# Kernel tuning notes

Measured on AMD Instinct MI355X. Metric: run time of the kernel, lower is better.

The kernel has to match this reference:

```python
import jax, jax.numpy as jnp
import numpy as np

D = 64      # hidden_dim
H = 4       # num_attention_heads
DH = D // H # head_dim
B = 64      # graphs per batch
SCALE = np.float32(np.sqrt(DH))


def _sage(x, edge, wl, bl, wr):
    # SAGEConv: lin_l(mean_j x_j) + lin_r(x_i); mean over incoming edges (dst = edge[1])
    src, dst = edge[0], edge[1]
    n = x.shape[0]
    agg = jax.ops.segment_sum(x[src], dst, num_segments=n)
    cnt = jax.ops.segment_sum(jnp.ones((edge.shape[1],), x.dtype), dst, num_segments=n)
    mean = agg / jnp.maximum(cnt, 1.0)[:, None]
    return mean @ wl + bl + x @ wr


def _cross_attn(xq, xk, w, b):
    # w: [3, D, D] stacked (Q, K, V) projections; b: [3, D]
    Q = (xq @ w[0] + b[0]).reshape(-1, H, DH)  # [Nq, H, DH]
    K = (xk @ w[1] + b[1]).reshape(-1, H, DH)  # [Nk, H, DH]
    V = (xk @ w[2] + b[2]).reshape(-1, H, DH)
    scores = jnp.einsum('qhd,khd->hqk', Q, K) / SCALE  # [H, Nq, Nk]
    wgt = jax.nn.softmax(scores, axis=-1)
    out = jnp.einsum('hqk,khd->qhd', wgt, V)
    return out.reshape(xq.shape[0], D)


def _segment_mean(x, seg, num):
    s = jax.ops.segment_sum(x, seg, num_segments=num)
    c = jax.ops.segment_sum(jnp.ones((x.shape[0],), x.dtype), seg, num_segments=num)
    return s / jnp.maximum(c, 1.0)[:, None]


def setup_inputs() -> dict:
    key = jax.random.key(0)
    ks = jax.random.split(key, 32)
    N_MOL, N_PROT, E_MOL, E_PROT = 2048, 8192, 32768, 131072
    MOL_IN, PROT_IN = 32, 64

    def lin(k, i, o, s=None):
        s = 1.0 / np.sqrt(i) if s is None else s
        return (jax.random.normal(k, (i, o), jnp.float32) * s)

    inp = {
        'x_mol': jax.random.normal(ks[0], (N_MOL, MOL_IN), jnp.float32),
        'x_prot': jax.random.normal(ks[1], (N_PROT, PROT_IN), jnp.float32),
        'm1_wl': lin(ks[2], MOL_IN, D), 'm1_bl': jnp.zeros((D,), jnp.float32), 'm1_wr': lin(ks[3], MOL_IN, D),
        'm2_wl': lin(ks[4], D, D), 'm2_bl': jnp.zeros((D,), jnp.float32), 'm2_wr': lin(ks[5], D, D),
        'p1_wl': lin(ks[6], PROT_IN, D), 'p1_bl': jnp.zeros((D,), jnp.float32), 'p1_wr': lin(ks[7], PROT_IN, D),
        'p2_wl': lin(ks[8], D, D), 'p2_bl': jnp.zeros((D,), jnp.float32), 'p2_wr': lin(ks[9], D, D),
        'amp_w': jax.random.normal(ks[10], (3, D, D), jnp.float32) / np.sqrt(D),
        'amp_b': jnp.zeros((3, D), jnp.float32),
        'apm_w': jax.random.normal(ks[11], (3, D, D), jnp.float32) / np.sqrt(D),
        'apm_b': jnp.zeros((3, D), jnp.float32),
        'fc1_w': lin(ks[12], 2 * D, D), 'fc1_b': jnp.zeros((D,), jnp.float32),
        'fc2_w': lin(ks[13], D, 1), 'fc2_b': jnp.zeros((1,), jnp.float32),
        'edge_mol': jax.random.randint(ks[14], (2, E_MOL), 0, N_MOL, jnp.int32),
        'edge_prot': jax.random.randint(ks[15], (2, E_PROT), 0, N_PROT, jnp.int32),
        'batch_mol': jnp.sort(jax.random.randint(ks[16], (N_MOL,), 0, B, jnp.int32)),
        'batch_prot': jnp.sort(jax.random.randint(ks[17], (N_PROT,), 0, B, jnp.int32)),
    }
    return inp


def reference(x_mol, x_prot,
              m1_wl, m1_bl, m1_wr, m2_wl, m2_bl, m2_wr,
              p1_wl, p1_bl, p1_wr, p2_wl, p2_bl, p2_wr,
              amp_w, amp_b, apm_w, apm_b,
              fc1_w, fc1_b, fc2_w, fc2_b,
              edge_mol, edge_prot, batch_mol, batch_prot):
    # two SAGE conv blocks per graph, ReLU after each (HeteroConv with one edge type)
    h_mol = jax.nn.relu(_sage(x_mol, edge_mol, m1_wl, m1_bl, m1_wr))
    h_mol = jax.nn.relu(_sage(h_mol, edge_mol, m2_wl, m2_bl, m2_wr))
    h_prot = jax.nn.relu(_sage(x_prot, edge_prot, p1_wl, p1_bl, p1_wr))
    h_prot = jax.nn.relu(_sage(h_prot, edge_prot, p2_wl, p2_bl, p2_wr))
    # cross attention (mol queries prot, prot queries mol) + residual
    h_mol_c = h_mol + _cross_attn(h_mol, h_prot, amp_w, amp_b)
    h_prot_c = h_prot + _cross_attn(h_prot, h_mol, apm_w, apm_b)
    # global mean pool per graph
    z_mol = _segment_mean(h_mol_c, batch_mol, B)    # [B, D]
    z_prot = _segment_mean(h_prot_c, batch_prot, B)  # [B, D]
    z = jnp.concatenate([z_mol, z_prot], axis=1)     # [B, 2D]
    x = jax.nn.relu(z @ fc1_w + fc1_b)
    out = jax.nn.sigmoid(x @ fc2_w + fc2_b)
    return out.squeeze(-1)  # [B]
```

## Files before the change

### kernel.cpp

```cpp
#include <hip/hip_runtime.h>
#include <math.h>

#define D 64
#define NB 64

typedef __attribute__((ext_vector_type(8))) short bf16x8;
typedef __attribute__((ext_vector_type(4))) float f32x4;
typedef __attribute__((ext_vector_type(16))) float f32x16;

#define M3(a, b, c) fmaxf(fmaxf((a), (b)), (c))

__device__ __forceinline__ unsigned short f2bf(float f) {
    unsigned u = __float_as_uint(f);
    u += 0x7FFF + ((u >> 16) & 1);
    return (unsigned short)(u >> 16);
}
__device__ __forceinline__ unsigned pk_bf16(float lo, float hi) {
    unsigned r;
    asm("v_cvt_pk_bf16_f32 %0, %1, %2" : "=v"(r) : "v"(lo), "v"(hi));
    return r;
}
__device__ __forceinline__ float fexp2(float x) {
    float r;
    asm("v_exp_f32 %0, %1" : "=v"(r) : "v"(x));
    return r;
}

__global__ void k_hist2(const int* __restrict__ em, int Em,
                        const int* __restrict__ ep, int Ep,
                        int* __restrict__ degm, int* __restrict__ degp) {
    int i = blockIdx.x * blockDim.x + threadIdx.x;
    if (i < Em) atomicAdd(&degm[em[Em + i]], 1);
    int j = i - Em;
    if (j >= 0 && j < Ep) atomicAdd(&degp[ep[Ep + j]], 1);
}

__global__ __launch_bounds__(256) void k_scan2(
        const int* __restrict__ degm, int Nm, int* __restrict__ rpm, int* __restrict__ curm,
        const int* __restrict__ degp, int Np, int* __restrict__ rpp, int* __restrict__ curp) {
    __shared__ int sdeg[8192];
    __shared__ int chunk[256];
    const int* deg = blockIdx.x ? degp : degm;
    int N = blockIdx.x ? Np : Nm;
    int* rowptr = blockIdx.x ? rpp : rpm;
    int* cursor = blockIdx.x ? curp : curm;
    int t = threadIdx.x;
    for (int i = t; i < N; i += 256) sdeg[i] = deg[i];
    __syncthreads();
    int C = (N + 255) / 256;
    int start = t * C;
    int sum = 0;
    for (int i = 0; i < C; ++i)
        if (start + i < N) sum += sdeg[start + i];
    chunk[t] = sum;
    __syncthreads();
    for (int ofs = 1; ofs < 256; ofs <<= 1) {
        int v = (t >= ofs) ? chunk[t - ofs] : 0;
        __syncthreads();
        chunk[t] += v;
        __syncthreads();
    }
    int base = (t == 0) ? 0 : chunk[t - 1];
    for (int i = 0; i < C && start + i < N; ++i) {
        rowptr[start + i] = base;
        cursor[start + i] = base;
        base += sdeg[start + i];
    }
    if (t == 255) rowptr[N] = base;
}

__global__ void k_scatter2(const int* __restrict__ em, int Em, int* __restrict__ curm,
                           int* __restrict__ csrm,
                           const int* __restrict__ ep, int Ep, int* __restrict__ curp,
                           int* __restrict__ csrp) {
    int i = blockIdx.x * blockDim.x + threadIdx.x;
    if (i < Em) {
        int s = em[i], d = em[Em + i];
        csrm[atomicAdd(&curm[d], 1)] = s;
    }
    int j = i - Em;
    if (j >= 0 && j < Ep) {
        int s = ep[j], d = ep[Ep + j];
        csrp[atomicAdd(&curp[d], 1)] = s;
    }
}

__global__ void k_bstart2(const int* __restrict__ bm, int Nm, int* __restrict__ bsM,
                          const int* __restrict__ bp, int Np, int* __restrict__ bsP) {
    int i = blockIdx.x * blockDim.x + threadIdx.x;
    if (i < Nm) {
        int cur = bm[i];
        int prev = (i == 0) ? -1 : bm[i - 1];
        for (int b = prev + 1; b <= cur; ++b) bsM[b] = i;
        if (i == Nm - 1)
            for (int b = cur + 1; b <= NB; ++b) bsM[b] = Nm;
    }
    int j = i - Nm;
    if (j >= 0 && j < Np) {
        int cur = bp[j];
        int prev = (j == 0) ? -1 : bp[j - 1];
        for (int b = prev + 1; b <= cur; ++b) bsP[b] = j;
        if (j == Np - 1)
            for (int b = cur + 1; b <= NB; ++b) bsP[b] = Np;
    }
}

template<int FIN>
__device__ __forceinline__ void gsage_body(
        const float* __restrict__ x, const int* __restrict__ rowptr,
        const int* __restrict__ csr, int N,
        const float* __restrict__ wl, const float* __restrict__ bl,
        const float* __restrict__ wr, float* __restrict__ out,
        int blk, float* __restrict__ swl, float* __restrict__ swr,
        float* __restrict__ sagg, float* __restrict__ sx) {
    for (int i = threadIdx.x; i < FIN * D; i += 256) { swl[i] = wl[i]; swr[i] = wr[i]; }
    int w = threadIdx.x >> 6;
    int lane = threadIdx.x & 63;
    int r = blk * 4 + w;
    if (r < N) {
        int e0 = rowptr[r], e1 = rowptr[r + 1];
        float inv = 1.0f / fmaxf((float)(e1 - e0), 1.0f);
        if (FIN == 64) {
            float a0 = 0.f, a1 = 0.f, a2 = 0.f, a3 = 0.f;
            int e = e0;
            for (; e + 3 < e1; e += 4) {
                a0 += x[(size_t)csr[e] * FIN + lane];
                a1 += x[(size_t)csr[e + 1] * FIN + lane];
                a2 += x[(size_t)csr[e + 2] * FIN + lane];
                a3 += x[(size_t)csr[e + 3] * FIN + lane];
            }
            for (; e < e1; ++e) a0 += x[(size_t)csr[e] * FIN + lane];
            sagg[w * 64 + lane] = ((a0 + a1) + (a2 + a3)) * inv;
            sx[w * 64 + lane] = x[(size_t)r * FIN + lane];
        } else {
            int f = lane & 31, half = lane >> 5;
            float a = 0.f;
            for (int e = e0 + half; e < e1; e += 2)
                a += x[(size_t)csr[e] * FIN + f];
            a += __shfl_xor(a, 32);
            if (half == 0) {
                sagg[w * 64 + f] = a * inv;
                sx[w * 64 + f] = x[(size_t)r * FIN + f];
            }
        }
    }
    __syncthreads();
    if (r >= N) return;
    int c = lane;
    float acc = bl[c];
    #pragma unroll 8
    for (int k = 0; k < FIN; ++k) {
        acc += sagg[w * 64 + k] * swl[k * D + c];
        acc += sx[w * 64 + k] * swr[k * D + c];
    }
    out[(size_t)r * D + c] = fmaxf(acc, 0.0f);
}

template<int FA, int FB>
__global__ __launch_bounds__(256) void k_gsage2(
        const float* __restrict__ xA, const int* __restrict__ rpA,
        const int* __restrict__ csrA, int NA,
        const float* __restrict__ wlA, const float* __restrict__ blA,
        const float* __restrict__ wrA, float* __restrict__ outA,
        const float* __restrict__ xB, const int* __restrict__ rpB,
        const int* __restrict__ csrB, int NB_,
        const float* __restrict__ wlB, const float* __restrict__ blB,
        const float* __restrict__ wrB, float* __restrict__ outB) {
    __shared__ float swl[64 * 64];
    __shared__ float swr[64 * 64];
    __shared__ float sagg[4 * 64];
    __shared__ float sx[4 * 64];
    int bA = NA / 4;
    if ((int)blockIdx.x < bA)
        gsage_body<FA>(xA, rpA, csrA, NA, wlA, blA, wrA, outA, blockIdx.x, swl, swr, sagg, sx);
    else
        gsage_body<FB>(xB, rpB, csrB, NB_, wlB, blB, wrB, outB, blockIdx.x - bA, swl, swr, sagg, sx);
}

__global__ __launch_bounds__(256) void k_qkv2(
        const float* __restrict__ xA, int NA, const float* __restrict__ xB, int NB_,
        const float* __restrict__ amp_w, const float* __restrict__ amp_b,
        const float* __restrict__ apm_w, const float* __restrict__ apm_b, float qs,
        unsigned short* __restrict__ QA, unsigned short* __restrict__ KA, unsigned short* __restrict__ VA,
        unsigned short* __restrict__ QB, unsigned short* __restrict__ KB, unsigned short* __restrict__ VB) {
    __shared__ float sq[D * D], sk[D * D], sv[D * D], sx[16 * D];
    int bA = NA / 16;
    const float *x, *wq, *bq, *wk, *bk, *wv, *bv;
    unsigned short *oq, *ok, *ov;
    int blk;
    if ((int)blockIdx.x < bA) {
        x = xA; blk = blockIdx.x;
        wq = amp_w;        bq = amp_b;
        wk = apm_w + 4096; bk = apm_b + 64;
        wv = apm_w + 8192; bv = apm_b + 128;
        oq = QA; ok = KA; ov = VA;
    } else {
        x = xB; blk = blockIdx.x - bA;
        wq = apm_w;        bq = apm_b;
        wk = amp_w + 4096; bk = amp_b + 64;
        wv = amp_w + 8192; bv = amp_b + 128;
        oq = QB; ok = KB; ov = VB;
    }
    for (int i = threadIdx.x; i < D * D; i += 256) { sq[i] = wq[i]; sk[i] = wk[i]; sv[i] = wv[i]; }
    int rbase = blk * 16;
    for (int i = threadIdx.x; i < 16 * D; i += 256) sx[i] = x[(size_t)rbase * D + i];
    __syncthreads();
    int c = threadIdx.x & 63;
    int r0 = (threadIdx.x >> 6) * 4;
    for (int rr = 0; rr < 4; ++rr) {
        int r = r0 + rr;
        float aq = bq[c], ak = bk[c], av = bv[c];
        #pragma unroll 8
        for (int k = 0; k < D; ++k) {
            float xv = sx[r * D + k];
            aq += xv * sq[k * D + c];
            ak += xv * sk[k * D + c];
            av += xv * sv[k * D + c];
        }
        size_t o = (size_t)(rbase + r) * D + c;
        oq[o] = f2bf(aq * qs);
        ok[o] = f2bf(ak);
        ov[o] = f2bf(av);
    }
}

__global__ void k_transp2(const unsigned short* __restrict__ inM, unsigned short* __restrict__ outM, int Nm,
                          const unsigned short* __restrict__ inP, unsigned short* __restrict__ outP, int Np) {
    __shared__ unsigned short tile[64][72];
    int bm = Nm >> 6;
    const unsigned short* in; unsigned short* out; int N;
    int blk = blockIdx.x;
    if (blk < bm) { in = inM; out = outM; N = Nm; }
    else { blk -= bm; in = inP; out = outP; N = Np; }
    int t = threadIdx.x;
    int rbase = blk * 64;
    {
        int r = t >> 2, c0 = (t & 3) * 16;
        const uint4* src = (const uint4*)(in + (size_t)(rbase + r) * 64 + c0);
        uint4 a = src[0], b = src[1];
        *(uint4*)(&tile[r][c0]) = a;
        *(uint4*)(&tile[r][c0 + 8]) = b;
    }
    __syncthreads();
    {
        int c = t >> 2, r0 = (t & 3) * 16;
        union { uint2 v2[4]; unsigned short s[16]; } u;
        #pragma unroll
        for (int i = 0; i < 16; ++i) u.s[i] = tile[r0 + i][c];
        int key0 = rbase + r0;
        int kc = key0 & ~31;
        int b16 = key0 & 16;
        unsigned short* op = out + (size_t)c * N;
        const int gmap[4] = {0, 8, 4, 12};
        #pragma unroll
        for (int b = 0; b < 4; ++b)
            *(uint2*)(op + kc + b16 + gmap[b]) = u.v2[b];
    }
    if (t < 8) {
        uint4 ones;
        ones.x = ones.y = ones.z = ones.w = 0x3F803F80u;
        *(uint4*)(out + (size_t)64 * N + rbase + t * 8) = ones;
    }
}

#define PVBLOCK(S, KB)                                                        \
    {                                                                         \
        float p[16];                                                          \
        _Pragma("unroll")                                                     \
        for (int i = 0; i < 16; ++i) p[i] = fexp2((S)[i]);                    \
        union { unsigned u[4]; bf16x8 v; } f1, f2;                            \
        f1.u[0] = pk_bf16(p[0], p[1]);   f1.u[1] = pk_bf16(p[2], p[3]);       \
        f1.u[2] = pk_bf16(p[4], p[5]);   f1.u[3] = pk_bf16(p[6], p[7]);       \
        f2.u[0] = pk_bf16(p[8], p[9]);   f2.u[1] = pk_bf16(p[10], p[11]);     \
        f2.u[2] = pk_bf16(p[12], p[13]); f2.u[3] = pk_bf16(p[14], p[15]);     \
        bf16x8 vb0 = *(const bf16x8*)(vbase + (KB) + half * 8);               \
        bf16x8 vb1 = *(const bf16x8*)(vbase + (KB) + 16 + half * 8);          \
        __builtin_amdgcn_s_setprio(1);                                        \
        o = __builtin_amdgcn_mfma_f32_32x32x16_bf16(f1.v, vb0, o, 0, 0, 0);   \
        o = __builtin_amdgcn_mfma_f32_32x32x16_bf16(f2.v, vb1, o, 0, 0, 0);   \
        __builtin_amdgcn_s_setprio(0);                                        \
    }

#define MAXTREE(cm, s0, s1)                                                   \
    {                                                                         \
        float c0 = M3(s0[0], s0[1], s0[2]);                                   \
        float c1 = M3(s0[3], s0[4], s0[5]);                                   \
        float c2 = M3(s0[6], s0[7], s0[8]);                                   \
        float c3 = M3(s0[9], s0[10], s0[11]);                                 \
        float c4 = M3(s0[12], s0[13], s0[14]);                                \
        float c5 = M3(s0[15], s1[0], s1[1]);                                  \
        float c6 = M3(s1[2], s1[3], s1[4]);                                   \
        float c7 = M3(s1[5], s1[6], s1[7]);                                   \
        float c8 = M3(s1[8], s1[9], s1[10]);                                  \
        float c9 = M3(s1[11], s1[12], s1[13]);                                \
        float ca = fmaxf(s1[14], s1[15]);                                     \
        float d0 = M3(c0, c1, c2);                                            \
        float d1 = M3(c3, c4, c5);                                            \
        float d2 = M3(c6, c7, c8);                                            \
        float d3 = M3(c9, ca, d0);                                            \
        cm = M3(d1, d2, d3);                                                  \
    }

__global__ __launch_bounds__(256) void k_attn2(
        const unsigned short* __restrict__ QmB, const unsigned short* __restrict__ KpB,
        const unsigned short* __restrict__ VpT, int Nm, int Np, int lsm,
        float* __restrict__ poM, float* __restrict__ pmM, float* __restrict__ plM,
        const unsigned short* __restrict__ QpB, const unsigned short* __restrict__ KmB,
        const unsigned short* __restrict__ VmT, int lsp,
        float* __restrict__ poP, float* __restrict__ pmP, float* __restrict__ plP) {
    const unsigned short *Q, *K, *Vt;
    int Nq, Nk, ls;
    float *po, *pm, *pl;
    if (blockIdx.y == 0) { Q = QmB; K = KpB; Vt = VpT; Nq = Nm; Nk = Np; ls = lsm; po = poM; pm = pmM; pl = plM; }
    else                 { Q = QpB; K = KmB; Vt = VmT; Nq = Np; Nk = Nm; ls = lsp; po = poP; pm = pmP; pl = plP; }
    int nqt = Nq >> 5;
    if ((int)blockIdx.x >= (nqt << ls)) return;
    const int qt = blockIdx.x >> ls;
    const int split = blockIdx.x & ((1 << ls) - 1);
    const int kchunk = Nk >> ls;
    const int h = threadIdx.x >> 6;
    const int lane = threadIdx.x & 63;
    const int cq = lane & 31;
    const int half = lane >> 5;
    const int h16 = h * 16;

    bf16x8 qb = *(const bf16x8*)(Q + ((size_t)(qt * 32 + cq) * D + h16 + half * 8));
    int drow = (cq < 16) ? (h16 + cq) : (cq == 16 ? 64 : h16 + 15);
    const unsigned short* vbase = Vt + (size_t)drow * Nk;

    f32x16 o, mC, zro;
    #pragma unroll
    for (int i = 0; i < 16; ++i) { o[i] = 0.f; zro[i] = 0.f; }
    float m;

    const int kstart = split * kchunk;
    {
        const int kb = kstart;
        bf16x8 ka0 = *(const bf16x8*)(K + ((size_t)(kb + cq) * D + h16 + half * 8));
        bf16x8 ka1 = *(const bf16x8*)(K + ((size_t)(kb + 32 + cq) * D + h16 + half * 8));
        f32x16 s0 = __builtin_amdgcn_mfma_f32_32x32x16_bf16(ka0, qb, zro, 0, 0, 0);
        f32x16 s1 = __builtin_amdgcn_mfma_f32_32x32x16_bf16(ka1, qb, zro, 0, 0, 0);
        float cm;
        MAXTREE(cm, s0, s1);
        #pragma unroll
        for (int off = 1; off < 64; off <<= 1) cm = fmaxf(cm, __shfl_xor(cm, off));
        m = cm;
        #pragma unroll
        for (int i = 0; i < 16; ++i) { s0[i] -= m; s1[i] -= m; mC[i] = -m; }
        PVBLOCK(s0, kb)
        PVBLOCK(s1, kb + 32)
    }
    for (int kb = kstart + 64; kb < kstart + kchunk; kb += 64) {
        bf16x8 ka0 = *(const bf16x8*)(K + ((size_t)(kb + cq) * D + h16 + half * 8));
        bf16x8 ka1 = *(const bf16x8*)(K + ((size_t)(kb + 32 + cq) * D + h16 + half * 8));
        f32x16 s0 = __builtin_amdgcn_mfma_f32_32x32x16_bf16(ka0, qb, mC, 0, 0, 0);
        f32x16 s1 = __builtin_amdgcn_mfma_f32_32x32x16_bf16(ka1, qb, mC, 0, 0, 0);
        float cm;
        MAXTREE(cm, s0, s1);
        if (__any(cm > 8.f)) {
            float cw = cm;
            #pragma unroll
            for (int off = 1; off < 64; off <<= 1) cw = fmaxf(cw, __shfl_xor(cw, off));
            float nm = fmaxf(m + cw, m);
            float sc = fexp2(m - nm);
            #pragma unroll
            for (int i = 0; i < 16; ++i) o[i] *= sc;
            float dl = nm - m;
            #pragma unroll
            for (int i = 0; i < 16; ++i) { s0[i] -= dl; s1[i] -= dl; mC[i] = -nm; }
            m = nm;
        }
        PVBLOCK(s0, kb)
        PVBLOCK(s1, kb + 32)
    }

    size_t pbase = (size_t)split * Nq + qt * 32;
    if (half == 0)
        pm[(pbase + cq) * 4 + h] = m;
    if (cq == 16) {
        #pragma unroll
        for (int r = 0; r < 16; ++r) {
            int qr = (r & 3) + 8 * (r >> 2) + 4 * half;
            pl[(pbase + qr) * 4 + h] = o[r];
        }
    }
    if (cq < 16) {
        #pragma unroll
        for (int r = 0; r < 16; ++r) {
            int qr = (r & 3) + 8 * (r >> 2) + 4 * half;
            po[(pbase + qr) * 64 + h16 + cq] = o[r];
        }
    }
}

template<int NS>
__device__ __forceinline__ void comb_body(
        const float* __restrict__ po, const float* __restrict__ pm,
        const float* __restrict__ pl, int Nq,
        const float* __restrict__ resid, float* __restrict__ outc, int i) {
    int q = i >> 4;
    int part = i & 15;
    int d0 = part * 4;
    int h = part >> 2;
    float pmv[NS], plv[NS];
    #pragma unroll
    for (int s = 0; s < NS; ++s) pmv[s] = pm[((size_t)s * Nq + q) * 4 + h];
    #pragma unroll
    for (int s = 0; s < NS; ++s) plv[s] = pl[((size_t)s * Nq + q) * 4 + h];
    float M = pmv[0];
    #pragma unroll
    for (int s = 1; s < NS; ++s) M = fmaxf(M, pmv[s]);
    float4 O = {0.f, 0.f, 0.f, 0.f};
    float L = 0.f;
    #pragma unroll
    for (int s = 0; s < NS; ++s) {
        float wgt = fexp2(pmv[s] - M);
        float4 pv = *(const float4*)(po + ((size_t)s * Nq + q) * 64 + d0);
        O.x += pv.x * wgt; O.y += pv.y * wgt; O.z += pv.z * wgt; O.w += pv.w * wgt;
        L += plv[s] * wgt;
    }
    float invL = 1.0f / L;
    float4 rv = *(const float4*)(resid + (size_t)q * 64 + d0);
    float4 res;
    res.x = rv.x + O.x * invL;
    res.y = rv.y + O.y * invL;
    res.z = rv.z + O.z * invL;
    res.w = rv.w + O.w * invL;
    *(float4*)(outc + (size_t)q * 64 + d0) = res;
}

template<int NSM, int NSP>
__global__ void k_comb2t(
        const float* __restrict__ poM, const float* __restrict__ pmM, const float* __restrict__ plM,
        int Nm, const float* __restrict__ residM, float* __restrict__ outM,
        const float* __restrict__ poP, const float* __restrict__ pmP, const float* __restrict__ plP,
        int Np, const float* __restrict__ residP, float* __restrict__ outP) {
    int idx = blockIdx.x * blockDim.x + threadIdx.x;
    int mtot = Nm * 16;
    if (idx < mtot)
        comb_body<NSM>(poM, pmM, plM, Nm, residM, outM, idx);
    else if (idx - mtot < Np * 16)
        comb_body<NSP>(poP, pmP, plP, Np, residP, outP, idx - mtot);
}

__global__ void k_comb2(
        const float* __restrict__ poM, const float* __restrict__ pmM, const float* __restrict__ plM,
        int nsM, int Nm, const float* __restrict__ residM, float* __restrict__ outM,
        const float* __restrict__ poP, const float* __restrict__ pmP, const float* __restrict__ plP,
        int nsP, int Np, const float* __restrict__ residP, float* __restrict__ outP) {
    int idx = blockIdx.x * blockDim.x + threadIdx.x;
    const float *po, *pm, *pl, *resid;
    float* outc;
    int ns, Nq, i;
    int mtot = Nm * 64;
    if (idx < mtot) {
        po = poM; pm = pmM; pl = plM; ns = nsM; Nq = Nm; resid = residM; outc = outM; i = idx;
    } else {
        i = idx - mtot;
        if (i >= Np * 64) return;
        po = poP; pm = pmP; pl = plP; ns = nsP; Nq = Np; resid = residP; outc = outP;
    }
    int q = i >> 6, d = i & 63, h = d >> 4;
    float M = -1e30f;
    for (int s = 0; s < ns; ++s)
        M = fmaxf(M, pm[((size_t)s * Nq + q) * 4 + h]);
    float O = 0.f, L = 0.f;
    for (int s = 0; s < ns; ++s) {
        float wgt = fexp2(pm[((size_t)s * Nq + q) * 4 + h] - M);
        O += po[((size_t)s * Nq + q) * 64 + d] * wgt;
        L += pl[((size_t)s * Nq + q) * 4 + h] * wgt;
    }
    outc[i] = resid[i] + O / L;
}

__global__ __launch_bounds__(256) void k_pool2(
        const float* __restrict__ hM, const int* __restrict__ bsM,
        const float* __restrict__ hP, const int* __restrict__ bsP,
        float* __restrict__ zsum, float* __restrict__ zcnt) {
    __shared__ float red[4][64];
    int b = blockIdx.x & 63;
    int isP = blockIdx.x >> 6;
    const float* h = isP ? hP : hM;
    const int* bs = isP ? bsP : bsM;
    int colOff = isP ? 64 : 0;
    int n0 = bs[b], n1 = bs[b + 1];
    int w = threadIdx.x >> 6, c = threadIdx.x & 63;
    float acc = 0.f;
    for (int n = n0 + w; n < n1; n += 4)
        acc += h[(size_t)n * 64 + c];
    red[w][c] = acc;
    __syncthreads();
    if (w == 0) {
        float s = (red[0][c] + red[1][c]) + (red[2][c] + red[3][c]);
        zsum[b * 128 + colOff + c] = s;
        if (c == 0) zcnt[b * 2 + isP] = (float)(n1 - n0);
    }
}

__global__ __launch_bounds__(256) void k_head2(
        const float* __restrict__ zsum, const float* __restrict__ zcnt,
        const float* __restrict__ fc1w, const float* __restrict__ fc1b,
        const float* __restrict__ fc2w, const float* __restrict__ fc2b,
        float* __restrict__ out) {
    int b = blockIdx.x * 4 + (threadIdx.x >> 6);
    int c = threadIdx.x & 63;
    float inv0 = 1.0f / fmaxf(zcnt[b * 2 + 0], 1.0f);
    float inv1 = 1.0f / fmaxf(zcnt[b * 2 + 1], 1.0f);
    float acc = fc1b[c];
    #pragma unroll 8
    for (int k = 0; k < 128; ++k) {
        float zv = zsum[b * 128 + k] * (k < 64 ? inv0 : inv1);
        acc += zv * fc1w[k * 64 + c];
    }
    float v = fmaxf(acc, 0.0f) * fc2w[c];
    #pragma unroll
    for (int off = 32; off > 0; off >>= 1) v += __shfl_xor(v, off);
    if (c == 0) out[b] = 1.0f / (1.0f + __expf(-(v + fc2b[0])));
}

extern "C" void kernel_launch(void* const* d_in, const int* in_sizes, int n_in,
                              void* d_out, int out_size, void* d_ws, size_t ws_size,
                              hipStream_t stream) {
    const float* x_mol  = (const float*)d_in[0];
    const float* x_prot = (const float*)d_in[1];
    const float* m1_wl = (const float*)d_in[2];
    const float* m1_bl = (const float*)d_in[3];
    const float* m1_wr = (const float*)d_in[4];
    const float* m2_wl = (const float*)d_in[5];
    const float* m2_bl = (const float*)d_in[6];
    const float* m2_wr = (const float*)d_in[7];
    const float* p1_wl = (const float*)d_in[8];
    const float* p1_bl = (const float*)d_in[9];
    const float* p1_wr = (const float*)d_in[10];
    const float* p2_wl = (const float*)d_in[11];
    const float* p2_bl = (const float*)d_in[12];
    const float* p2_wr = (const float*)d_in[13];
    const float* amp_w = (const float*)d_in[14];
    const float* amp_b = (const float*)d_in[15];
    const float* apm_w = (const float*)d_in[16];
    const float* apm_b = (const float*)d_in[17];
    const float* fc1_w = (const float*)d_in[18];
    const float* fc1_b = (const float*)d_in[19];
    const float* fc2_w = (const float*)d_in[20];
    const float* fc2_b = (const float*)d_in[21];
    const int* edge_mol  = (const int*)d_in[22];
    const int* edge_prot = (const int*)d_in[23];
    const int* batch_mol  = (const int*)d_in[24];
    const int* batch_prot = (const int*)d_in[25];
    float* out = (float*)d_out;

    const int N_MOL  = in_sizes[0] / 32;
    const int N_PROT = in_sizes[1] / 64;
    const int E_MOL  = in_sizes[22] / 2;
    const int E_PROT = in_sizes[23] / 2;

    char* base = (char*)d_ws;
    size_t off = 0;
    auto alloc = [&](size_t bytes) -> void* {
        void* p = base + off;
        off = (off + bytes + 255) & ~(size_t)255;
        return p;
    };
    float* h_mol1   = (float*)alloc((size_t)N_MOL * D * sizeof(float));
    float* h_mol2   = (float*)alloc((size_t)N_MOL * D * sizeof(float));
    float* h_prot1  = (float*)alloc((size_t)N_PROT * D * sizeof(float));
    float* h_prot2  = (float*)alloc((size_t)N_PROT * D * sizeof(float));
    float* h_mol_c  = (float*)alloc((size_t)N_MOL * D * sizeof(float));
    float* h_prot_c = (float*)alloc((size_t)N_PROT * D * sizeof(float));
    float* zsum     = (float*)alloc((NB * 128 + NB * 2) * sizeof(float));
    float* zcnt     = zsum + NB * 128;
    unsigned short* Qm_b = (unsigned short*)alloc((size_t)N_MOL * D * 2);
    unsigned short* Km_b = (unsigned short*)alloc((size_t)N_MOL * D * 2);
    unsigned short* Vm_b = (unsigned short*)alloc((size_t)N_MOL * D * 2);
    unsigned short* Vm_t = (unsigned short*)alloc((size_t)N_MOL * (D + 1) * 2);
    unsigned short* Qp_b = (unsigned short*)alloc((size_t)N_PROT * D * 2);
    unsigned short* Kp_b = (unsigned short*)alloc((size_t)N_PROT * D * 2);
    unsigned short* Vp_b = (unsigned short*)alloc((size_t)N_PROT * D * 2);
    unsigned short* Vp_t = (unsigned short*)alloc((size_t)N_PROT * (D + 1) * 2);
    int* deg      = (int*)alloc(((size_t)N_MOL + N_PROT) * sizeof(int));
    int* deg_m    = deg;
    int* deg_p    = deg + N_MOL;
    int* rp_m     = (int*)alloc(((size_t)N_MOL + 1) * sizeof(int));
    int* cur_m    = (int*)alloc((size_t)N_MOL * sizeof(int));
    int* csr_m    = (int*)alloc((size_t)E_MOL * sizeof(int));
    int* rp_p     = (int*)alloc(((size_t)N_PROT + 1) * sizeof(int));
    int* cur_p    = (int*)alloc((size_t)N_PROT * sizeof(int));
    int* csr_p    = (int*)alloc((size_t)E_PROT * sizeof(int));
    int* bsM      = (int*)alloc((NB + 1) * sizeof(int));
    int* bsP      = (int*)alloc((NB + 1) * sizeof(int));

    int nsm = 16; while (nsm > 1 && (N_PROT % (64 * nsm))) nsm >>= 1;
    int nsp = 4;  while (nsp > 1 && (N_MOL % (64 * nsp)))  nsp >>= 1;
    int lsm = 31 - __builtin_clz(nsm);
    int lsp = 31 - __builtin_clz(nsp);
    float* poM = (float*)alloc((size_t)nsm * N_MOL * 64 * sizeof(float));
    float* pmM = (float*)alloc((size_t)nsm * N_MOL * 4 * sizeof(float));
    float* plM = (float*)alloc((size_t)nsm * N_MOL * 4 * sizeof(float));
    float* poP = (float*)alloc((size_t)nsp * N_PROT * 64 * sizeof(float));
    float* pmP = (float*)alloc((size_t)nsp * N_PROT * 4 * sizeof(float));
    float* plP = (float*)alloc((size_t)nsp * N_PROT * 4 * sizeof(float));

    const int BLK = 256;
    dim3 blk(BLK);
    const float QS = 0.25f * 1.4426950408889634f;

    hipMemsetAsync(deg, 0, ((size_t)N_MOL + N_PROT) * sizeof(int), stream);
    int Etot = E_MOL + E_PROT;
    k_hist2<<<(Etot + BLK - 1) / BLK, blk, 0, stream>>>(edge_mol, E_MOL, edge_prot, E_PROT, deg_m, deg_p);
    k_bstart2<<<(N_MOL + N_PROT + BLK - 1) / BLK, blk, 0, stream>>>(
        batch_mol, N_MOL, bsM, batch_prot, N_PROT, bsP);
    k_scan2<<<2, blk, 0, stream>>>(deg_m, N_MOL, rp_m, cur_m, deg_p, N_PROT, rp_p, cur_p);
    k_scatter2<<<(Etot + BLK - 1) / BLK, blk, 0, stream>>>(edge_mol, E_MOL, cur_m, csr_m,
                                                           edge_prot, E_PROT, cur_p, csr_p);

    k_gsage2<32, 64><<<N_MOL / 4 + N_PROT / 4, blk, 0, stream>>>(
        x_mol,  rp_m, csr_m, N_MOL,  m1_wl, m1_bl, m1_wr, h_mol1,
        x_prot, rp_p, csr_p, N_PROT, p1_wl, p1_bl, p1_wr, h_prot1);
    k_gsage2<64, 64><<<N_MOL / 4 + N_PROT / 4, blk, 0, stream>>>(
        h_mol1,  rp_m, csr_m, N_MOL,  m2_wl, m2_bl, m2_wr, h_mol2,
        h_prot1, rp_p, csr_p, N_PROT, p2_wl, p2_bl, p2_wr, h_prot2);

    k_qkv2<<<N_MOL / 16 + N_PROT / 16, blk, 0, stream>>>(
        h_mol2, N_MOL, h_prot2, N_PROT, amp_w, amp_b, apm_w, apm_b, QS,
        Qm_b, Km_b, Vm_b, Qp_b, Kp_b, Vp_b);

    k_transp2<<<N_MOL / 64 + N_PROT / 64, blk, 0, stream>>>(Vm_b, Vm_t, N_MOL, Vp_b, Vp_t, N_PROT);

    int gxm = (N_MOL / 32) * nsm;
    int gxp = (N_PROT / 32) * nsp;
    int gx = gxm > gxp ? gxm : gxp;
    k_attn2<<<dim3(gx, 2), blk, 0, stream>>>(
        Qm_b, Kp_b, Vp_t, N_MOL, N_PROT, lsm, poM, pmM, plM,
        Qp_b, Km_b, Vm_t, lsp, poP, pmP, plP);

    if (nsm == 16 && nsp == 4) {
        int tot = (N_MOL + N_PROT) * 16;
        k_comb2t<16, 4><<<(tot + BLK - 1) / BLK, blk, 0, stream>>>(
            poM, pmM, plM, N_MOL, h_mol2, h_mol_c,
            poP, pmP, plP, N_PROT, h_prot2, h_prot_c);
    } else {
        k_comb2<<<((N_MOL + N_PROT) * 64 + BLK - 1) / BLK, blk, 0, stream>>>(
            poM, pmM, plM, nsm, N_MOL, h_mol2, h_mol_c,
            poP, pmP, plP, nsp, N_PROT, h_prot2, h_prot_c);
    }

    k_pool2<<<128, blk, 0, stream>>>(h_mol_c, bsM, h_prot_c, bsP, zsum, zcnt);

    k_head2<<<16, blk, 0, stream>>>(zsum, zcnt, fc1_w, fc1_b, fc2_w, fc2_b, out);
}
```

Measured before the change: 175.2 us.

## Fuse histogram and batch-start kernels; restructure attention loop to 32-key blocks

Merges the degree histogram and batch-start kernels into one launch, removing one kernel launch. Rewrites the attention inner loop to process 32 keys per iteration instead of 64, dropping the trick of folding the negative running max into the MFMA accumulator. The max is now subtracted explicitly before exp2, and the rescale threshold is compared against m+8 directly. This halves the register footprint of the score tiles but doubles loop iterations and adds explicit subtractions.

```diff
diff --git a/kernel.cpp b/kernel.cpp
--- a/kernel.cpp
+++ b/kernel.cpp
@@ -26,13 +26,30 @@
     return r;
 }
 
-__global__ void k_hist2(const int* __restrict__ em, int Em,
+__global__ void k_prep2(const int* __restrict__ em, int Em,
                         const int* __restrict__ ep, int Ep,
-                        int* __restrict__ degm, int* __restrict__ degp) {
+                        int* __restrict__ degm, int* __restrict__ degp,
+                        const int* __restrict__ bm, int Nm, int* __restrict__ bsM,
+                        const int* __restrict__ bp, int Np, int* __restrict__ bsP) {
     int i = blockIdx.x * blockDim.x + threadIdx.x;
     if (i < Em) atomicAdd(&degm[em[Em + i]], 1);
     int j = i - Em;
     if (j >= 0 && j < Ep) atomicAdd(&degp[ep[Ep + j]], 1);
+    if (i < Nm) {
+        int cur = bm[i];
+        int prev = (i == 0) ? -1 : bm[i - 1];
+        for (int b = prev + 1; b <= cur; ++b) bsM[b] = i;
+        if (i == Nm - 1)
+            for (int b = cur + 1; b <= NB; ++b) bsM[b] = Nm;
+    }
+    int j2 = i - Nm;
+    if (j2 >= 0 && j2 < Np) {
+        int cur = bp[j2];
+        int prev = (j2 == 0) ? -1 : bp[j2 - 1];
+        for (int b = prev + 1; b <= cur; ++b) bsP[b] = j2;
+        if (j2 == Np - 1)
+            for (int b = cur + 1; b <= NB; ++b) bsP[b] = Np;
+    }
 }
 
 __global__ __launch_bounds__(256) void k_scan2(
@@ -82,26 +99,6 @@
     if (j >= 0 && j < Ep) {
         int s = ep[j], d = ep[Ep + j];
         csrp[atomicAdd(&curp[d], 1)] = s;
-    }
-}
-
-__global__ void k_bstart2(const int* __restrict__ bm, int Nm, int* __restrict__ bsM,
-                          const int* __restrict__ bp, int Np, int* __restrict__ bsP) {
-    int i = blockIdx.x * blockDim.x + threadIdx.x;
-    if (i < Nm) {
-        int cur = bm[i];
-        int prev = (i == 0) ? -1 : bm[i - 1];
-        for (int b = prev + 1; b <= cur; ++b) bsM[b] = i;
-        if (i == Nm - 1)
-            for (int b = cur + 1; b <= NB; ++b) bsM[b] = Nm;
-    }
-    int j = i - Nm;
-    if (j >= 0 && j < Np) {
-        int cur = bp[j];
-        int prev = (j == 0) ? -1 : bp[j - 1];
-        for (int b = prev + 1; b <= cur; ++b) bsP[b] = j;
-        if (j == Np - 1)
-            for (int b = cur + 1; b <= NB; ++b) bsP[b] = Np;
     }
 }
 
@@ -263,16 +260,25 @@
     }
 }
 
-#define PVBLOCK(S, KB)                                                        \
+#define MAXTREE16(cm, s)                                                      \
     {                                                                         \
-        float p[16];                                                          \
-        _Pragma("unroll")                                                     \
-        for (int i = 0; i < 16; ++i) p[i] = fexp2((S)[i]);                    \
+        float c0 = M3(s[0], s[1], s[2]);                                      \
+        float c1 = M3(s[3], s[4], s[5]);                                      \
+        float c2 = M3(s[6], s[7], s[8]);                                      \
+        float c3 = M3(s[9], s[10], s[11]);                                    \
+        float c4 = M3(s[12], s[13], s[14]);                                   \
+        float d0 = M3(c0, c1, c2);                                            \
+        float d1 = M3(c3, c4, s[15]);                                         \
+        cm = fmaxf(d0, d1);                                                   \
+    }
+
+#define PVPACK(S, KB)                                                         \
+    {                                                                         \
         union { unsigned u[4]; bf16x8 v; } f1, f2;                            \
-        f1.u[0] = pk_bf16(p[0], p[1]);   f1.u[1] = pk_bf16(p[2], p[3]);       \
-        f1.u[2] = pk_bf16(p[4], p[5]);   f1.u[3] = pk_bf16(p[6], p[7]);       \
-        f2.u[0] = pk_bf16(p[8], p[9]);   f2.u[1] = pk_bf16(p[10], p[11]);     \
-        f2.u[2] = pk_bf16(p[12], p[13]); f2.u[3] = pk_bf16(p[14], p[15]);     \
+        f1.u[0] = pk_bf16((S)[0], (S)[1]);   f1.u[1] = pk_bf16((S)[2], (S)[3]);  \
+        f1.u[2] = pk_bf16((S)[4], (S)[5]);   f1.u[3] = pk_bf16((S)[6], (S)[7]);  \
+        f2.u[0] = pk_bf16((S)[8], (S)[9]);   f2.u[1] = pk_bf16((S)[10], (S)[11]);\
+        f2.u[2] = pk_bf16((S)[12], (S)[13]); f2.u[3] = pk_bf16((S)[14], (S)[15]);\
         bf16x8 vb0 = *(const bf16x8*)(vbase + (KB) + half * 8);               \
         bf16x8 vb1 = *(const bf16x8*)(vbase + (KB) + 16 + half * 8);          \
         __builtin_amdgcn_s_setprio(1);                                        \
@@ -281,27 +287,7 @@
         __builtin_amdgcn_s_setprio(0);                                        \
     }
 
-#define MAXTREE(cm, s0, s1)                                                   \
-    {                                                                         \
-        float c0 = M3(s0[0], s0[1], s0[2]);                                   \
-        float c1 = M3(s0[3], s0[4], s0[5]);                                   \
-        float c2 = M3(s0[6], s0[7], s0[8]);                                   \
-        float c3 = M3(s0[9], s0[10], s0[11]);                                 \
-        float c4 = M3(s0[12], s0[13], s0[14]);                                \
-        float c5 = M3(s0[15], s1[0], s1[1]);                                  \
-        float c6 = M3(s1[2], s1[3], s1[4]);                                   \
-        float c7 = M3(s1[5], s1[6], s1[7]);                                   \
-        float c8 = M3(s1[8], s1[9], s1[10]);                                  \
-        float c9 = M3(s1[11], s1[12], s1[13]);                                \
-        float ca = fmaxf(s1[14], s1[15]);                                     \
-        float d0 = M3(c0, c1, c2);                                            \
-        float d1 = M3(c3, c4, c5);                                            \
-        float d2 = M3(c6, c7, c8);                                            \
-        float d3 = M3(c9, ca, d0);                                            \
-        cm = M3(d1, d2, d3);                                                  \
-    }
-
-__global__ __launch_bounds__(256) void k_attn2(
+__global__ __launch_bounds__(256) void k_attn3(
         const unsigned short* __restrict__ QmB, const unsigned short* __restrict__ KpB,
         const unsigned short* __restrict__ VpT, int Nm, int Np, int lsm,
         float* __restrict__ poM, float* __restrict__ pmM, float* __restrict__ plM,
@@ -328,50 +314,42 @@
     int drow = (cq < 16) ? (h16 + cq) : (cq == 16 ? 64 : h16 + 15);
     const unsigned short* vbase = Vt + (size_t)drow * Nk;
 
-    f32x16 o, mC, zro;
+    f32x16 o, zro;
     #pragma unroll
     for (int i = 0; i < 16; ++i) { o[i] = 0.f; zro[i] = 0.f; }
     float m;
 
     const int kstart = split * kchunk;
     {
-        const int kb = kstart;
-        bf16x8 ka0 = *(const bf16x8*)(K + ((size_t)(kb + cq) * D + h16 + half * 8));
-        bf16x8 ka1 = *(const bf16x8*)(K + ((size_t)(kb + 32 + cq) * D + h16 + half * 8));
-        f32x16 s0 = __builtin_amdgcn_mfma_f32_32x32x16_bf16(ka0, qb, zro, 0, 0, 0);
-        f32x16 s1 = __builtin_amdgcn_mfma_f32_32x32x16_bf16(ka1, qb, zro, 0, 0, 0);
+        bf16x8 ka = *(const bf16x8*)(K + ((size_t)(kstart + cq) * D + h16 + half * 8));
+        f32x16 s = __builtin_amdgcn_mfma_f32_32x32x16_bf16(ka, qb, zro, 0, 0, 0);
         float cm;
-        MAXTREE(cm, s0, s1);
+        MAXTREE16(cm, s);
         #pragma unroll
         for (int off = 1; off < 64; off <<= 1) cm = fmaxf(cm, __shfl_xor(cm, off));
         m = cm;
         #pragma unroll
-        for (int i = 0; i < 16; ++i) { s0[i] -= m; s1[i] -= m; mC[i] = -m; }
-        PVBLOCK(s0, kb)
-        PVBLOCK(s1, kb + 32)
-    }
-    for (int kb = kstart + 64; kb < kstart + kchunk; kb += 64) {
-        bf16x8 ka0 = *(const bf16x8*)(K + ((size_t)(kb + cq) * D + h16 + half * 8));
-        bf16x8 ka1 = *(const bf16x8*)(K + ((size_t)(kb + 32 + cq) * D + h16 + half * 8));
-        f32x16 s0 = __builtin_amdgcn_mfma_f32_32x32x16_bf16(ka0, qb, mC, 0, 0, 0);
-        f32x16 s1 = __builtin_amdgcn_mfma_f32_32x32x16_bf16(ka1, qb, mC, 0, 0, 0);
+        for (int i = 0; i < 16; ++i) s[i] = fexp2(s[i] - m);
+        PVPACK(s, kstart)
+    }
+    for (int kb = kstart + 32; kb < kstart + kchunk; kb += 32) {
+        bf16x8 ka = *(const bf16x8*)(K + ((size_t)(kb + cq) * D + h16 + half * 8));
+        f32x16 s = __builtin_amdgcn_mfma_f32_32x32x16_bf16(ka, qb, zro, 0, 0, 0);
         float cm;
-        MAXTREE(cm, s0, s1);
-        if (__any(cm > 8.f)) {
+        MAXTREE16(cm, s);
+        if (__any(cm > m + 8.f)) {
             float cw = cm;
             #pragma unroll
             for (int off = 1; off < 64; off <<= 1) cw = fmaxf(cw, __shfl_xor(cw, off));
-            float nm = fmaxf(m + cw, m);
+            float nm = fmaxf(cw, m);
             float sc = fexp2(m - nm);
             #pragma unroll
             for (int i = 0; i < 16; ++i) o[i] *= sc;
-            float dl = nm - m;
-            #pragma unroll
-            for (int i = 0; i < 16; ++i) { s0[i] -= dl; s1[i] -= dl; mC[i] = -nm; }
             m = nm;
         }
-        PVBLOCK(s0, kb)
-        PVBLOCK(s1, kb + 32)
+        #pragma unroll
+        for (int i = 0; i < 16; ++i) s[i] = fexp2(s[i] - m);
+        PVPACK(s, kb)
     }
 
     size_t pbase = (size_t)split * Nq + qt * 32;
@@ -606,8 +584,8 @@
 
     hipMemsetAsync(deg, 0, ((size_t)N_MOL + N_PROT) * sizeof(int), stream);
     int Etot = E_MOL + E_PROT;
-    k_hist2<<<(Etot + BLK - 1) / BLK, blk, 0, stream>>>(edge_mol, E_MOL, edge_prot, E_PROT, deg_m, deg_p);
-    k_bstart2<<<(N_MOL + N_PROT + BLK - 1) / BLK, blk, 0, stream>>>(
+    k_prep2<<<(Etot + BLK - 1) / BLK, blk, 0, stream>>>(
+        edge_mol, E_MOL, edge_prot, E_PROT, deg_m, deg_p,
         batch_mol, N_MOL, bsM, batch_prot, N_PROT, bsP);
     k_scan2<<<2, blk, 0, stream>>>(deg_m, N_MOL, rp_m, cur_m, deg_p, N_PROT, rp_p, cur_p);
     k_scatter2<<<(Etot + BLK - 1) / BLK, blk, 0, stream>>>(edge_mol, E_MOL, cur_m, csr_m,
@@ -629,7 +607,7 @@
     int gxm = (N_MOL / 32) * nsm;
     int gxp = (N_PROT / 32) * nsp;
     int gx = gxm > gxp ? gxm : gxp;
-    k_attn2<<<dim3(gx, 2), blk, 0, stream>>>(
+    k_attn3<<<dim3(gx, 2), blk, 0, stream>>>(
         Qm_b, Kp_b, Vp_t, N_MOL, N_PROT, lsm, poM, pmM, plM,
         Qp_b, Km_b, Vm_t, lsp, poP, pmP, plP);
 
```

After: 174.5 us. Within noise of the previous version (-0.4%).
